# Performance work log

Measured on AMD Instinct MI355X. Metric: run time of the kernel, lower is better.

## Reference

```python
import jax, jax.numpy as jnp
import numpy as np

B, S, IN, OUT, L = 8, 2048, 4096, 64, 16

def setup_inputs() -> dict:
    key = jax.random.key(0)
    k1, k2, k3 = jax.random.split(key, 3)
    x = jax.random.normal(k1, (B, S, IN), dtype=jnp.float32)
    adapter_ids = jax.random.randint(k2, (B,), 0, L)
    weight = jax.random.normal(k3, (L, OUT, IN), dtype=jnp.float32) * 0.02
    return {"x": x, "adapter_ids": adapter_ids, "weight": weight}

def reference(x, adapter_ids, weight):
    # Gather one [OUT, IN] weight per batch element, then per-sample linear.
    # Equivalent to the torch loop: stack_i F.linear(x[i], weight[adapter_ids[i]]).
    w = weight[adapter_ids]                      # [B, OUT, IN]
    return jnp.einsum('bsi,boi->bso', x, w)      # [B, S, OUT]
```

## Files before the change

### kernel.cpp

```cpp
#include <hip/hip_runtime.h>
#include <stdint.h>

#define NB   8
#define NS   2048
#define NIN  4096
#define NOUT 64
#define NL   16

constexpr int MT = 16;
constexpr int KT = 128;
constexpr int NT = NIN / KT;

typedef __attribute__((ext_vector_type(8))) short  s16x8;
typedef __attribute__((ext_vector_type(4))) float  f32x4;
typedef __attribute__((ext_vector_type(4))) float  fv4;
typedef __attribute__((ext_vector_type(4))) __bf16 bf16x4;

__device__ __forceinline__ s16x8 cvt8(float4 a, float4 b) {
    fv4 va = {a.x, a.y, a.z, a.w};
    fv4 vb = {b.x, b.y, b.z, b.w};
    union { struct { bf16x4 lo, hi; } h; s16x8 s; } u;
    u.h.lo = __builtin_convertvector(va, bf16x4);
    u.h.hi = __builtin_convertvector(vb, bf16x4);
    return u.s;
}

__global__ __launch_bounds__(256) void convert_w_kernel(const float* __restrict__ w,
                                                        unsigned short* __restrict__ o) {
    size_t i = ((size_t)blockIdx.x * 256 + threadIdx.x) * 8;
    const float4* src = (const float4*)(w + i);
    *(s16x8*)(o + i) = cvt8(src[0], src[1]);
}

template <bool WBF16>
__global__ __launch_bounds__(256, 4) void mll_kernel(const float* __restrict__ x,
                                                     const int* __restrict__ ids,
                                                     const void* __restrict__ wsel,
                                                     float* __restrict__ out) {
    __shared__ __align__(16) unsigned short xs[2 * MT * KT];

    const int bx   = blockIdx.x;
    const int b    = bx & 7;
    const int mt   = bx >> 3;
    const int aid  = ids[b];
    const int t    = threadIdx.x;
    const int lane = t & 63;
    const int wv   = t >> 6;
    const int l15  = lane & 15;
    const int lk   = lane >> 4;

    const int srow = t >> 4;
    const int sq   = t & 15;
    const float* gsrc = x + ((size_t)(b * NS + mt * MT + srow)) * NIN + sq * 8;
    const int woff = srow * KT + ((sq ^ srow) * 8);

    int roff[4];
#pragma unroll
    for (int s = 0; s < 4; ++s) roff[s] = l15 * KT + (((s * 4 + lk) ^ l15) * 8);

    const unsigned short* wb16 = nullptr;
    const float*          wb32 = nullptr;
    if (WBF16) wb16 = (const unsigned short*)wsel + ((size_t)(aid * NOUT + wv * 16 + l15)) * NIN + lk * 8;
    else       wb32 = (const float*)wsel          + ((size_t)(aid * NOUT + wv * 16 + l15)) * NIN + lk * 8;

    f32x4 acc = {0.f, 0.f, 0.f, 0.f};

#define LOAD_B(dst, tt)                                                        \
    if (WBF16) {                                                               \
        _Pragma("unroll")                                                      \
        for (int s = 0; s < 4; ++s)                                            \
            dst[s] = *(const s16x8*)(wb16 + (size_t)(tt) * KT + s * 32);       \
    } else {                                                                   \
        _Pragma("unroll")                                                      \
        for (int s = 0; s < 4; ++s) {                                          \
            const float4* _wp = (const float4*)(wb32 + (size_t)(tt) * KT + s * 32); \
            dst[s] = cvt8(_wp[0], _wp[1]);                                     \
        }                                                                      \
    }

    {
        const float4* g0 = (const float4*)gsrc;
        *(s16x8*)(xs + woff) = cvt8(g0[0], g0[1]);
    }
    const float4* g1 = (const float4*)(gsrc + KT);
    float4 r0 = g1[0], r1 = g1[1];
    s16x8 bcur[4], bnext[4];
    LOAD_B(bcur, 0);
    __syncthreads();

    for (int tile = 0; tile < NT; ++tile) {
        const int p = tile & 1;

        const int pt = (tile + 2 < NT) ? (tile + 2) : (NT - 1);
        const float4* gn = (const float4*)(gsrc + (size_t)pt * KT);
        float4 n0 = gn[0], n1 = gn[1];

        const int bt = (tile + 1 < NT) ? (tile + 1) : (NT - 1);
        LOAD_B(bnext, bt);

        const unsigned short* buf = xs + p * (MT * KT);
#pragma unroll
        for (int s = 0; s < 4; ++s) {
            s16x8 af = *(const s16x8*)(buf + roff[s]);
            acc = __builtin_amdgcn_mfma_f32_16x16x32_bf16(af, bcur[s], acc, 0, 0, 0);
        }

        if (tile + 1 < NT) {
            *(s16x8*)(xs + (1 - p) * (MT * KT) + woff) = cvt8(r0, r1);
        }
        r0 = n0; r1 = n1;
#pragma unroll
        for (int s = 0; s < 4; ++s) bcur[s] = bnext[s];
        __syncthreads();
    }
#undef LOAD_B

    float* ob = out + ((size_t)(b * NS + mt * MT)) * NOUT + wv * 16 + l15;
#pragma unroll
    for (int r = 0; r < 4; ++r) {
        ob[(size_t)(lk * 4 + r) * NOUT] = acc[r];
    }
}

extern "C" void kernel_launch(void* const* d_in, const int* in_sizes, int n_in,
                              void* d_out, int out_size, void* d_ws, size_t ws_size,
                              hipStream_t stream) {
    const float* x   = (const float*)d_in[0];
    const int*   ids = (const int*)d_in[1];
    const float* w   = (const float*)d_in[2];
    float*       out = (float*)d_out;

    const size_t wbytes = (size_t)NL * NOUT * NIN * sizeof(unsigned short);
    const int grid = NB * (NS / MT);

    if (ws_size >= wbytes) {
        unsigned short* wbf = (unsigned short*)d_ws;
        const int n = NL * NOUT * NIN;
        convert_w_kernel<<<n / (256 * 8), 256, 0, stream>>>(w, wbf);
        mll_kernel<true><<<grid, 256, 0, stream>>>(x, ids, wbf, out);
    } else {
        mll_kernel<false><<<grid, 256, 0, stream>>>(x, ids, w, out);
    }
}
```

Baseline: 375.5 us.

## Split K across two blocks with atomic accumulation and drop weight pre-conversion

```diff
diff --git a/kernel.cpp b/kernel.cpp
--- a/kernel.cpp
+++ b/kernel.cpp
@@ -7,9 +7,10 @@
 #define NOUT 64
 #define NL   16
 
-constexpr int MT = 16;
-constexpr int KT = 128;
-constexpr int NT = NIN / KT;
+constexpr int MT    = 16;
+constexpr int KT    = 128;
+constexpr int KHALF = NIN / 2;
+constexpr int NT    = KHALF / KT;
 
 typedef __attribute__((ext_vector_type(8))) short  s16x8;
 typedef __attribute__((ext_vector_type(4))) float  f32x4;
@@ -25,58 +26,36 @@
     return u.s;
 }
 
-__global__ __launch_bounds__(256) void convert_w_kernel(const float* __restrict__ w,
-                                                        unsigned short* __restrict__ o) {
-    size_t i = ((size_t)blockIdx.x * 256 + threadIdx.x) * 8;
-    const float4* src = (const float4*)(w + i);
-    *(s16x8*)(o + i) = cvt8(src[0], src[1]);
-}
-
-template <bool WBF16>
-__global__ __launch_bounds__(256, 4) void mll_kernel(const float* __restrict__ x,
+__global__ __launch_bounds__(256, 5) void mll_kernel(const float* __restrict__ x,
                                                      const int* __restrict__ ids,
-                                                     const void* __restrict__ wsel,
+                                                     const float* __restrict__ w,
                                                      float* __restrict__ out) {
     __shared__ __align__(16) unsigned short xs[2 * MT * KT];
 
     const int bx   = blockIdx.x;
     const int b    = bx & 7;
-    const int mt   = bx >> 3;
+    const int mt   = (bx >> 3) & 127;
+    const int kh   = bx >> 10;
     const int aid  = ids[b];
     const int t    = threadIdx.x;
     const int lane = t & 63;
     const int wv   = t >> 6;
     const int l15  = lane & 15;
     const int lk   = lane >> 4;
+    const int koff = kh * KHALF;
 
     const int srow = t >> 4;
     const int sq   = t & 15;
-    const float* gsrc = x + ((size_t)(b * NS + mt * MT + srow)) * NIN + sq * 8;
+    const float* gsrc = x + ((size_t)(b * NS + mt * MT + srow)) * NIN + koff + sq * 8;
     const int woff = srow * KT + ((sq ^ srow) * 8);
 
     int roff[4];
 #pragma unroll
     for (int s = 0; s < 4; ++s) roff[s] = l15 * KT + (((s * 4 + lk) ^ l15) * 8);
 
-    const unsigned short* wb16 = nullptr;
-    const float*          wb32 = nullptr;
-    if (WBF16) wb16 = (const unsigned short*)wsel + ((size_t)(aid * NOUT + wv * 16 + l15)) * NIN + lk * 8;
-    else       wb32 = (const float*)wsel          + ((size_t)(aid * NOUT + wv * 16 + l15)) * NIN + lk * 8;
+    const float* wb = w + ((size_t)(aid * NOUT + wv * 16 + l15)) * NIN + koff + lk * 8;
 
     f32x4 acc = {0.f, 0.f, 0.f, 0.f};
-
-#define LOAD_B(dst, tt)                                                        \
-    if (WBF16) {                                                               \
-        _Pragma("unroll")                                                      \
-        for (int s = 0; s < 4; ++s)                                            \
-            dst[s] = *(const s16x8*)(wb16 + (size_t)(tt) * KT + s * 32);       \
-    } else {                                                                   \
-        _Pragma("unroll")                                                      \
-        for (int s = 0; s < 4; ++s) {                                          \
-            const float4* _wp = (const float4*)(wb32 + (size_t)(tt) * KT + s * 32); \
-            dst[s] = cvt8(_wp[0], _wp[1]);                                     \
-        }                                                                      \
-    }
 
     {
         const float4* g0 = (const float4*)gsrc;
@@ -84,8 +63,16 @@
     }
     const float4* g1 = (const float4*)(gsrc + KT);
     float4 r0 = g1[0], r1 = g1[1];
-    s16x8 bcur[4], bnext[4];
-    LOAD_B(bcur, 0);
+
+    float4 braw[8];
+#pragma unroll
+    for (int s = 0; s < 4; ++s) {
+        const float4* wp = (const float4*)(wb + s * 32);
+        braw[2 * s] = wp[0]; braw[2 * s + 1] = wp[1];
+    }
+    s16x8 bcur[4];
+#pragma unroll
+    for (int s = 0; s < 4; ++s) bcur[s] = cvt8(braw[2 * s], braw[2 * s + 1]);
     __syncthreads();
 
     for (int tile = 0; tile < NT; ++tile) {
@@ -96,7 +83,11 @@
         float4 n0 = gn[0], n1 = gn[1];
 
         const int bt = (tile + 1 < NT) ? (tile + 1) : (NT - 1);
-        LOAD_B(bnext, bt);
+#pragma unroll
+        for (int s = 0; s < 4; ++s) {
+            const float4* wp = (const float4*)(wb + (size_t)bt * KT + s * 32);
+            braw[2 * s] = wp[0]; braw[2 * s + 1] = wp[1];
+        }
 
         const unsigned short* buf = xs + p * (MT * KT);
 #pragma unroll
@@ -109,16 +100,16 @@
             *(s16x8*)(xs + (1 - p) * (MT * KT) + woff) = cvt8(r0, r1);
         }
         r0 = n0; r1 = n1;
+
 #pragma unroll
-        for (int s = 0; s < 4; ++s) bcur[s] = bnext[s];
+        for (int s = 0; s < 4; ++s) bcur[s] = cvt8(braw[2 * s], braw[2 * s + 1]);
         __syncthreads();
     }
-#undef LOAD_B
 
     float* ob = out + ((size_t)(b * NS + mt * MT)) * NOUT + wv * 16 + l15;
 #pragma unroll
     for (int r = 0; r < 4; ++r) {
-        ob[(size_t)(lk * 4 + r) * NOUT] = acc[r];
+        unsafeAtomicAdd(&ob[(size_t)(lk * 4 + r) * NOUT], acc[r]);
     }
 }
 
@@ -130,15 +121,8 @@
     const float* w   = (const float*)d_in[2];
     float*       out = (float*)d_out;
 
-    const size_t wbytes = (size_t)NL * NOUT * NIN * sizeof(unsigned short);
-    const int grid = NB * (NS / MT);
+    hipMemsetAsync(d_out, 0, (size_t)out_size * sizeof(float), stream);
 
-    if (ws_size >= wbytes) {
-        unsigned short* wbf = (unsigned short*)d_ws;
-        const int n = NL * NOUT * NIN;
-        convert_w_kernel<<<n / (256 * 8), 256, 0, stream>>>(w, wbf);
-        mll_kernel<true><<<grid, 256, 0, stream>>>(x, ids, wbf, out);
-    } else {
-        mll_kernel<false><<<grid, 256, 0, stream>>>(x, ids, w, out);
-    }
+    const int grid = NB * (NS / MT) * 2;
+    mll_kernel<<<grid, 256, 0, stream>>>(x, ids, w, out);
 }
```

New measurement: 429.6 us. 14.4% more time.
